# Kernel tuning notes

Hardware: AMD Instinct MI355X
Metric: run time of the kernel (lower is better)

The kernel has to match this reference:

```python
import jax, jax.numpy as jnp
import numpy as np

EPS = 1e-12  # F.normalize default eps

def setup_inputs() -> dict:
    key = jax.random.key(0)
    k1, k2, k3, k4, k5, k6 = jax.random.split(key, 6)
    N, F, T = 2000, 64, 24
    x = jax.random.normal(k1, (N, F, T), dtype=jnp.float32)
    adj_norm = jax.random.uniform(k2, (N, N), dtype=jnp.float32)
    weight = jax.random.normal(k3, (N, F, F), dtype=jnp.float32) / (F * F)
    Wq = jax.random.normal(k4, (F, F), dtype=jnp.float32) * 0.1
    Wk = jax.random.normal(k5, (F, F), dtype=jnp.float32) * 0.1
    Wv = jax.random.normal(k6, (F, F), dtype=jnp.float32) * 0.1
    return {"x": x, "adj_norm": adj_norm, "weight": weight, "Wq": Wq, "Wk": Wk, "Wv": Wv}

def reference(x, adj_norm, weight, Wq, Wk, Wv):
    # x: (N, F, T)
    N, F, T = x.shape
    # ---- Spatial_Attention_layer ----
    z = jnp.transpose(x, (2, 0, 1))                     # (T, N, F)
    nrm = jnp.sqrt(jnp.sum(z * z, axis=2, keepdims=True))
    z1 = z / jnp.maximum(nrm, EPS)
    score = jnp.einsum('tnf,tmf->tnm', z1, z1)          # (T, N, N)
    score = jax.nn.softmax(score, axis=-1)
    adj = adj_norm[None, :, :] * score                  # (T, N, N)
    # ---- CrossAttention fusion (shape-preserving self-attn over T) ----
    xt = jnp.transpose(x, (0, 2, 1))                    # (N, T, F)
    q = xt @ Wq
    k = xt @ Wk
    v = xt @ Wv
    a = jax.nn.softmax(jnp.einsum('ntf,nsf->nts', q, k) / jnp.sqrt(jnp.float32(F)), axis=-1)
    xf = jnp.einsum('nts,nsf->ntf', a, v)               # (N, T, F)
    xp = jnp.transpose(xf, (1, 0, 2))                   # (T, N, F) == x.permute(2,0,1)
    # ---- einsum('phh,bhi->bhi', adj, x): multiply by sum_p diag(adj[p]) ----
    diag_adj = jnp.sum(jnp.diagonal(adj, axis1=1, axis2=2), axis=0)      # (N,)
    # ---- einsum('bhi,pii->bhi', y, weight): multiply by sum_p diag(weight[p]) ----
    diag_w = jnp.sum(jnp.diagonal(weight, axis1=1, axis2=2), axis=0)     # (F,)
    out = xp * diag_adj[None, :, None] * diag_w[None, None, :]           # (T, N, F)
    return jnp.transpose(out, (1, 2, 0))                # (N, F, T)
```

## Files before the change

### kernel.cpp

```cpp
#include <hip/hip_runtime.h>
#include <hip/hip_bf16.h>

#define N_   2000
#define NP   2048
#define F_   64
#define T_   24

typedef short  v8s  __attribute__((ext_vector_type(8)));
typedef float  v4f  __attribute__((ext_vector_type(4)));
typedef unsigned short v4us __attribute__((ext_vector_type(4)));

__device__ __forceinline__ unsigned short f2bf(float f) {
  unsigned int u = __float_as_uint(f);
  u += 0x7fffu + ((u >> 16) & 1u);
  return (unsigned short)(u >> 16);
}

__global__ __launch_bounds__(256) void prep(const float* __restrict__ x,
                                            const float* __restrict__ w,
                                            const float* __restrict__ wq,
                                            const float* __restrict__ wk,
                                            const float* __restrict__ wv,
                                            unsigned short* __restrict__ zb,
                                            float* __restrict__ dw,
                                            unsigned short* __restrict__ wT) {
  __shared__ float xs[F_ * 25];
  __shared__ float red[4];
  int b = blockIdx.x;
  int tid = threadIdx.x, wave = tid >> 6, lane = tid & 63;

  if (b < NP) {
    int n = b;
    if (n >= N_) {
      for (int t = wave; t < T_; t += 4) zb[(t * NP + n) * F_ + lane] = 0;
      return;
    }
    const float* xn = x + n * (F_ * T_);
    for (int i = tid; i < F_ * T_; i += 256)
      xs[(i / T_) * 25 + (i % T_)] = xn[i];
    __syncthreads();
    for (int t = wave; t < T_; t += 4) {
      float v = xs[lane * 25 + t];
      float ss = v * v;
      #pragma unroll
      for (int m = 1; m < 64; m <<= 1) ss += __shfl_xor(ss, m);
      float nrm = fmaxf(sqrtf(ss), 1e-12f);
      zb[(t * NP + n) * F_ + lane] = f2bf(v / nrm);
    }
  } else if (b < NP + 64) {
    int f = b - NP;
    float s = 0.f;
    for (int p = tid; p < N_; p += 256) s += w[p * (F_ * F_) + f * (F_ + 1)];
    #pragma unroll
    for (int m = 1; m < 64; m <<= 1) s += __shfl_xor(s, m);
    if (lane == 0) red[wave] = s;
    __syncthreads();
    if (tid == 0) dw[f] = red[0] + red[1] + red[2] + red[3];
  } else {
    for (int i = tid; i < 3 * 4096; i += 256) {
      int m = i >> 12, r = i & 4095;
      const float* src = (m == 0) ? wq : (m == 1) ? wk : wv;
      int fi = r >> 6, fo = r & 63;
      wT[m * 4096 + fo * 64 + fi] = f2bf(src[r]);
    }
  }
}

__global__ __launch_bounds__(256) void gram_expsum(const unsigned short* __restrict__ zb,
                                                   float* __restrict__ partial) {
  int rb = blockIdx.x, cb = blockIdx.y, t = blockIdx.z;
  int wave = threadIdx.x >> 6, lane = threadIdx.x & 63;
  int lr = lane & 15, lk = (lane >> 4) * 8;
  const unsigned short* z = zb + t * (NP * F_);
  int r0 = rb * 256 + wave * 64;

  v8s a[4][2];
  #pragma unroll
  for (int rg = 0; rg < 4; rg++)
    #pragma unroll
    for (int kb = 0; kb < 2; kb++)
      a[rg][kb] = *(const v8s*)(z + (r0 + rg * 16 + lr) * F_ + kb * 32 + lk);

  float acc[16];
  #pragma unroll
  for (int i = 0; i < 16; i++) acc[i] = 0.f;

  int c0 = cb * 512, c1 = (cb == 3) ? N_ : c0 + 512;
  const unsigned short* bp = z + (c0 + lr) * F_ + lk;
  v4f cz = {0.f, 0.f, 0.f, 0.f};
  const float INV_E = 0.36787944117144233f;

  for (int c = c0; c < c1; c += 16) {
    v8s b0 = *(const v8s*)(bp);
    v8s b1 = *(const v8s*)(bp + 32);
    bp += 16 * F_;
    #pragma unroll
    for (int rg = 0; rg < 4; rg++) {
      v4f C = __builtin_amdgcn_mfma_f32_16x16x32_bf16(a[rg][0], b0, cz, 0, 0, 0);
      C = __builtin_amdgcn_mfma_f32_16x16x32_bf16(a[rg][1], b1, C, 0, 0, 0);
      #pragma unroll
      for (int i = 0; i < 4; i++)
        acc[rg * 4 + i] = fmaf(__expf(C[i]), INV_E, acc[rg * 4 + i]);
    }
  }
  #pragma unroll
  for (int i = 0; i < 16; i++) {
    acc[i] += __shfl_xor(acc[i], 1);
    acc[i] += __shfl_xor(acc[i], 2);
    acc[i] += __shfl_xor(acc[i], 4);
    acc[i] += __shfl_xor(acc[i], 8);
  }
  if (lr == 0) {
    float* ps = partial + (cb * T_ + t) * NP;
    #pragma unroll
    for (int rg = 0; rg < 4; rg++)
      #pragma unroll
      for (int i = 0; i < 4; i++)
        ps[r0 + rg * 16 + (lane >> 4) * 4 + i] = acc[rg * 4 + i];
  }
}

__global__ __launch_bounds__(256) void cross_attn(const float* __restrict__ x,
                                                  const unsigned short* __restrict__ wT,
                                                  const float* __restrict__ adj,
                                                  const float* __restrict__ partial,
                                                  const float* __restrict__ dw_g,
                                                  float* __restrict__ out) {
  __shared__ __align__(16) unsigned short lds[4 * 8192];
  int wave = threadIdx.x >> 6, lane = threadIdx.x & 63;
  int n = blockIdx.x * 4 + wave;
  unsigned short* xt = lds + wave * 8192;
  unsigned short* q  = xt + 2048;
  unsigned short* k  = xt + 4096;
  unsigned short* vT = xt + 6144;
  unsigned short* p  = xt;
  int lr = lane & 15, lk = (lane >> 4) * 8;
  int row0q = (lane >> 4) * 4;
  v4f cz = {0.f, 0.f, 0.f, 0.f};

  float invsum = 0.f;
  if (lane < T_) {
    float s = 0.f;
    #pragma unroll
    for (int cb = 0; cb < 4; cb++) s += partial[(cb * T_ + lane) * NP + n];
    invsum = 1.0f / s;
  }
  #pragma unroll
  for (int m = 1; m < 64; m <<= 1) invsum += __shfl_xor(invsum, m);
  float dadj = adj[n * (N_ + 1)] * invsum;

  const float* xn = x + n * (F_ * T_);
  #pragma unroll
  for (int j = 0; j < 24; j++) {
    int i = j * 64 + lane;
    float v = xn[i];
    xt[(i % T_) * 64 + (i / T_)] = f2bf(v);
  }
  { v8s z8 = {0,0,0,0,0,0,0,0}; *(v8s*)(xt + 24 * 64 + lane * 8) = z8; }

  v8s xa[2][2];
  #pragma unroll
  for (int rt = 0; rt < 2; rt++)
    #pragma unroll
    for (int kb = 0; kb < 2; kb++)
      xa[rt][kb] = *(const v8s*)(xt + (rt * 16 + lr) * 64 + kb * 32 + lk);

  #pragma unroll
  for (int m = 0; m < 3; m++) {
    const unsigned short* wt = wT + m * 4096;
    unsigned short* dst = (m == 0) ? q : k;
    #pragma unroll
    for (int ct = 0; ct < 4; ct++) {
      v8s b0 = *(const v8s*)(wt + (ct * 16 + lr) * 64 + lk);
      v8s b1 = *(const v8s*)(wt + (ct * 16 + lr) * 64 + 32 + lk);
      int col = ct * 16 + lr;
      #pragma unroll
      for (int rt = 0; rt < 2; rt++) {
        v4f C = __builtin_amdgcn_mfma_f32_16x16x32_bf16(xa[rt][0], b0, cz, 0, 0, 0);
        C = __builtin_amdgcn_mfma_f32_16x16x32_bf16(xa[rt][1], b1, C, 0, 0, 0);
        int r0 = rt * 16 + row0q;
        if (m < 2) {
          #pragma unroll
          for (int i = 0; i < 4; i++) dst[(r0 + i) * 64 + col] = f2bf(C[i]);
        } else {
          v4us pk = { f2bf(C[0]), f2bf(C[1]), f2bf(C[2]), f2bf(C[3]) };
          *(v4us*)(vT + col * 32 + r0) = pk;
        }
      }
    }
  }

  v8s qa[2][2];
  #pragma unroll
  for (int rt = 0; rt < 2; rt++)
    #pragma unroll
    for (int kb = 0; kb < 2; kb++)
      qa[rt][kb] = *(const v8s*)(q + (rt * 16 + lr) * 64 + kb * 32 + lk);

  float ev[2][2][4];
  #pragma unroll
  for (int ct = 0; ct < 2; ct++) {
    v8s b0 = *(const v8s*)(k + (ct * 16 + lr) * 64 + lk);
    v8s b1 = *(const v8s*)(k + (ct * 16 + lr) * 64 + 32 + lk);
    int col = ct * 16 + lr;
    #pragma unroll
    for (int rt = 0; rt < 2; rt++) {
      v4f C = __builtin_amdgcn_mfma_f32_16x16x32_bf16(qa[rt][0], b0, cz, 0, 0, 0);
      C = __builtin_amdgcn_mfma_f32_16x16x32_bf16(qa[rt][1], b1, C, 0, 0, 0);
      #pragma unroll
      for (int i = 0; i < 4; i++)
        ev[ct][rt][i] = (col < T_) ? __expf(C[i] * 0.125f) : 0.0f;
    }
  }
  #pragma unroll
  for (int rt = 0; rt < 2; rt++)
    #pragma unroll
    for (int i = 0; i < 4; i++) {
      float r = ev[0][rt][i] + ev[1][rt][i];
      r += __shfl_xor(r, 1); r += __shfl_xor(r, 2);
      r += __shfl_xor(r, 4); r += __shfl_xor(r, 8);
      float inv = 1.0f / r;
      int row = rt * 16 + row0q + i;
      p[row * 32 + lr]      = f2bf(ev[0][rt][i] * inv);
      p[row * 32 + 16 + lr] = f2bf(ev[1][rt][i] * inv);
    }

  v8s pa[2];
  #pragma unroll
  for (int rt = 0; rt < 2; rt++)
    pa[rt] = *(const v8s*)(p + (rt * 16 + lr) * 32 + lk);
  float* outn = out + n * (F_ * T_);
  #pragma unroll
  for (int ct = 0; ct < 4; ct++) {
    v8s vb = *(const v8s*)(vT + (ct * 16 + lr) * 32 + lk);
    float sc = dadj * dw_g[ct * 16 + lr];
    #pragma unroll
    for (int rt = 0; rt < 2; rt++) {
      v4f C = __builtin_amdgcn_mfma_f32_16x16x32_bf16(pa[rt], vb, cz, 0, 0, 0);
      int r0 = rt * 16 + row0q;
      if (r0 < T_) {
        v4f o;
        #pragma unroll
        for (int i = 0; i < 4; i++) o[i] = C[i] * sc;
        *(v4f*)(outn + (ct * 16 + lr) * T_ + r0) = o;
      }
    }
  }
}

extern "C" void kernel_launch(void* const* d_in, const int* in_sizes, int n_in,
                              void* d_out, int out_size, void* d_ws, size_t ws_size,
                              hipStream_t stream) {
  const float* x   = (const float*)d_in[0];
  const float* adj = (const float*)d_in[1];
  const float* w   = (const float*)d_in[2];
  const float* wq  = (const float*)d_in[3];
  const float* wk  = (const float*)d_in[4];
  const float* wv  = (const float*)d_in[5];
  float* out = (float*)d_out;

  char* ws = (char*)d_ws;
  unsigned short* zb      = (unsigned short*)ws;
  float*          partial = (float*)(ws + 6291456);
  float*          dw      = (float*)(ws + 6291456 + 786432);
  unsigned short* wT      = (unsigned short*)(ws + 6291456 + 786432 + 256);

  hipLaunchKernelGGL(prep,        dim3(NP + 64 + 1), dim3(256), 0, stream,
                     x, w, wq, wk, wv, zb, dw, wT);
  hipLaunchKernelGGL(gram_expsum, dim3(8, 4, 24),    dim3(256), 0, stream, zb, partial);
  hipLaunchKernelGGL(cross_attn,  dim3(500),         dim3(256), 0, stream,
                     x, wT, adj, partial, dw, out);
}
```

Measured before the change: 153.9 us.

## Exploit Gram symmetry with upper-triangular tiles and exp2 via prescaled inputs

The Gram-softmax row-sum kernel now computes only upper-triangular 256x256 tile pairs. Off-diagonal tiles contribute both row and column sums through atomicAdd into a zeroed rowsum buffer, which roughly halves the MFMA and exp work. The normalized inputs are prescaled by sqrt(log2 e) so that exp2 replaces expf, and the dropped 1/e shift is restored as a factor of e in the final scale. The cost is atomic contention, an extra zeroing pass in prep, and some unused padded columns in the last tile.

```diff
diff --git a/kernel.cpp b/kernel.cpp
--- a/kernel.cpp
+++ b/kernel.cpp
@@ -8,7 +8,11 @@
 
 typedef short  v8s  __attribute__((ext_vector_type(8)));
 typedef float  v4f  __attribute__((ext_vector_type(4)));
+typedef float  v4f_ __attribute__((ext_vector_type(4)));
 typedef unsigned short v4us __attribute__((ext_vector_type(4)));
+
+#define ALPHA 1.2011224087864498f
+#define E_CONST 2.718281828459045f
 
 __device__ __forceinline__ unsigned short f2bf(float f) {
   unsigned int u = __float_as_uint(f);
@@ -23,7 +27,8 @@
                                             const float* __restrict__ wv,
                                             unsigned short* __restrict__ zb,
                                             float* __restrict__ dw,
-                                            unsigned short* __restrict__ wT) {
+                                            unsigned short* __restrict__ wT,
+                                            float* __restrict__ rowsum) {
   __shared__ float xs[F_ * 25];
   __shared__ float red[4];
   int b = blockIdx.x;
@@ -45,7 +50,7 @@
       #pragma unroll
       for (int m = 1; m < 64; m <<= 1) ss += __shfl_xor(ss, m);
       float nrm = fmaxf(sqrtf(ss), 1e-12f);
-      zb[(t * NP + n) * F_ + lane] = f2bf(v / nrm);
+      zb[(t * NP + n) * F_ + lane] = f2bf(v / nrm * ALPHA);
     }
   } else if (b < NP + 64) {
     int f = b - NP;
@@ -56,23 +61,30 @@
     if (lane == 0) red[wave] = s;
     __syncthreads();
     if (tid == 0) dw[f] = red[0] + red[1] + red[2] + red[3];
-  } else {
+  } else if (b == NP + 64) {
     for (int i = tid; i < 3 * 4096; i += 256) {
       int m = i >> 12, r = i & 4095;
       const float* src = (m == 0) ? wq : (m == 1) ? wk : wv;
       int fi = r >> 6, fo = r & 63;
       wT[m * 4096 + fo * 64 + fi] = f2bf(src[r]);
     }
+  } else {
+    int blk = b - (NP + 65);
+    v4f_ z4 = {0.f, 0.f, 0.f, 0.f};
+    *(v4f_*)(rowsum + blk * 1024 + tid * 4) = z4;
   }
 }
 
 __global__ __launch_bounds__(256) void gram_expsum(const unsigned short* __restrict__ zb,
-                                                   float* __restrict__ partial) {
-  int rb = blockIdx.x, cb = blockIdx.y, t = blockIdx.z;
+                                                   float* __restrict__ rowsum) {
+  int p = blockIdx.x, t = blockIdx.y;
+  int bi = 0;
+  while (p >= 8 - bi) { p -= 8 - bi; bi++; }
+  int bj = bi + p;
   int wave = threadIdx.x >> 6, lane = threadIdx.x & 63;
   int lr = lane & 15, lk = (lane >> 4) * 8;
   const unsigned short* z = zb + t * (NP * F_);
-  int r0 = rb * 256 + wave * 64;
+  int r0 = bi * 256 + wave * 64;
 
   v8s a[4][2];
   #pragma unroll
@@ -81,49 +93,59 @@
     for (int kb = 0; kb < 2; kb++)
       a[rg][kb] = *(const v8s*)(z + (r0 + rg * 16 + lr) * F_ + kb * 32 + lk);
 
-  float acc[16];
-  #pragma unroll
-  for (int i = 0; i < 16; i++) acc[i] = 0.f;
-
-  int c0 = cb * 512, c1 = (cb == 3) ? N_ : c0 + 512;
+  float racc[16];
+  #pragma unroll
+  for (int i = 0; i < 16; i++) racc[i] = 0.f;
+
+  int c0 = bj * 256;
+  int c1 = (c0 + 256 > N_) ? N_ : c0 + 256;
   const unsigned short* bp = z + (c0 + lr) * F_ + lk;
   v4f cz = {0.f, 0.f, 0.f, 0.f};
-  const float INV_E = 0.36787944117144233f;
+  float* rs = rowsum + t * NP;
+  bool offd = (bi != bj);
 
   for (int c = c0; c < c1; c += 16) {
     v8s b0 = *(const v8s*)(bp);
     v8s b1 = *(const v8s*)(bp + 32);
     bp += 16 * F_;
+    float colacc = 0.f;
     #pragma unroll
     for (int rg = 0; rg < 4; rg++) {
       v4f C = __builtin_amdgcn_mfma_f32_16x16x32_bf16(a[rg][0], b0, cz, 0, 0, 0);
       C = __builtin_amdgcn_mfma_f32_16x16x32_bf16(a[rg][1], b1, C, 0, 0, 0);
       #pragma unroll
+      for (int i = 0; i < 4; i++) {
+        float e = __builtin_amdgcn_exp2f(C[i]);
+        racc[rg * 4 + i] += e;
+        colacc += e;
+      }
+    }
+    if (offd) {
+      colacc += __shfl_xor(colacc, 16);
+      colacc += __shfl_xor(colacc, 32);
+      if ((lane >> 4) == 0) atomicAdd(&rs[c + lr], colacc);
+    }
+  }
+  #pragma unroll
+  for (int i = 0; i < 16; i++) {
+    racc[i] += __shfl_xor(racc[i], 1);
+    racc[i] += __shfl_xor(racc[i], 2);
+    racc[i] += __shfl_xor(racc[i], 4);
+    racc[i] += __shfl_xor(racc[i], 8);
+  }
+  if (lr == 0) {
+    #pragma unroll
+    for (int rg = 0; rg < 4; rg++)
+      #pragma unroll
       for (int i = 0; i < 4; i++)
-        acc[rg * 4 + i] = fmaf(__expf(C[i]), INV_E, acc[rg * 4 + i]);
-    }
-  }
-  #pragma unroll
-  for (int i = 0; i < 16; i++) {
-    acc[i] += __shfl_xor(acc[i], 1);
-    acc[i] += __shfl_xor(acc[i], 2);
-    acc[i] += __shfl_xor(acc[i], 4);
-    acc[i] += __shfl_xor(acc[i], 8);
-  }
-  if (lr == 0) {
-    float* ps = partial + (cb * T_ + t) * NP;
-    #pragma unroll
-    for (int rg = 0; rg < 4; rg++)
-      #pragma unroll
-      for (int i = 0; i < 4; i++)
-        ps[r0 + rg * 16 + (lane >> 4) * 4 + i] = acc[rg * 4 + i];
+        atomicAdd(&rs[r0 + rg * 16 + (lane >> 4) * 4 + i], racc[rg * 4 + i]);
   }
 }
 
 __global__ __launch_bounds__(256) void cross_attn(const float* __restrict__ x,
                                                   const unsigned short* __restrict__ wT,
                                                   const float* __restrict__ adj,
-                                                  const float* __restrict__ partial,
+                                                  const float* __restrict__ rowsum,
                                                   const float* __restrict__ dw_g,
                                                   float* __restrict__ out) {
   __shared__ __align__(16) unsigned short lds[4 * 8192];
@@ -139,15 +161,10 @@
   v4f cz = {0.f, 0.f, 0.f, 0.f};
 
   float invsum = 0.f;
-  if (lane < T_) {
-    float s = 0.f;
-    #pragma unroll
-    for (int cb = 0; cb < 4; cb++) s += partial[(cb * T_ + lane) * NP + n];
-    invsum = 1.0f / s;
-  }
+  if (lane < T_) invsum = 1.0f / rowsum[lane * NP + n];
   #pragma unroll
   for (int m = 1; m < 64; m <<= 1) invsum += __shfl_xor(invsum, m);
-  float dadj = adj[n * (N_ + 1)] * invsum;
+  float dadj = adj[n * (N_ + 1)] * E_CONST * invsum;
 
   const float* xn = x + n * (F_ * T_);
   #pragma unroll
@@ -260,14 +277,14 @@
   float* out = (float*)d_out;
 
   char* ws = (char*)d_ws;
-  unsigned short* zb      = (unsigned short*)ws;
-  float*          partial = (float*)(ws + 6291456);
-  float*          dw      = (float*)(ws + 6291456 + 786432);
-  unsigned short* wT      = (unsigned short*)(ws + 6291456 + 786432 + 256);
-
-  hipLaunchKernelGGL(prep,        dim3(NP + 64 + 1), dim3(256), 0, stream,
-                     x, w, wq, wk, wv, zb, dw, wT);
-  hipLaunchKernelGGL(gram_expsum, dim3(8, 4, 24),    dim3(256), 0, stream, zb, partial);
-  hipLaunchKernelGGL(cross_attn,  dim3(500),         dim3(256), 0, stream,
-                     x, wT, adj, partial, dw, out);
-}
+  unsigned short* zb     = (unsigned short*)ws;
+  float*          rowsum = (float*)(ws + 6291456);
+  float*          dw     = (float*)(ws + 6291456 + 196608);
+  unsigned short* wT     = (unsigned short*)(ws + 6291456 + 196608 + 256);
+
+  hipLaunchKernelGGL(prep,        dim3(NP + 64 + 1 + 48), dim3(256), 0, stream,
+                     x, w, wq, wk, wv, zb, dw, wT, rowsum);
+  hipLaunchKernelGGL(gram_expsum, dim3(36, 24),           dim3(256), 0, stream, zb, rowsum);
+  hipLaunchKernelGGL(cross_attn,  dim3(500),              dim3(256), 0, stream,
+                     x, wT, adj, rowsum, dw, out);
+}
```

Measured after the change: 149.4 us (median of 2 runs). -2.9%, faster.
